# Kernel tuning notes

Measured on AMD Instinct MI355X. Metric: run time of the kernel, lower is better.

Reference implementation:

```python
import jax, jax.numpy as jnp
import numpy as np

DIN = 2048
DOUT = 2048
NUM_HEADS = 16
HEAD_DIM = DIN // NUM_HEADS  # 128
BLOCK_SIZE = 2048
ROPE_THETA = 10000.0


def precompute_freqs(block_size, head_dim):
    inv_freq = 1.0 / (ROPE_THETA ** (jnp.arange(0, head_dim, 2, dtype=jnp.float32) / head_dim))
    t = jnp.arange(block_size, dtype=jnp.float32)
    freqs = jnp.outer(t, inv_freq)  # [S, head_dim//2]
    return jnp.cos(freqs), jnp.sin(freqs)


def apply_rotary_emb(x, cos, sin):
    # x: [B, S, H, D]; cos/sin: [S, D//2]
    xr = x.reshape(*x.shape[:-1], -1, 2)  # pairs of consecutive dims (complex view)
    x1, x2 = xr[..., 0], xr[..., 1]
    c = cos[None, :, None, :]
    s = sin[None, :, None, :]
    o1 = x1 * c - x2 * s
    o2 = x1 * s + x2 * c
    return jnp.stack([o1, o2], axis=-1).reshape(x.shape)


def setup_inputs() -> dict:
    key = jax.random.key(0)
    k1, k2, k3 = jax.random.split(key, 3)
    x = jax.random.normal(k1, (2, 2048, DIN), dtype=jnp.float32)
    Wqkv = jax.random.normal(k2, (DIN, 3 * DOUT), dtype=jnp.float32) * (DIN ** -0.5)
    Wproj = jax.random.normal(k3, (DIN, DOUT), dtype=jnp.float32) * (DIN ** -0.5)
    return {"x": x, "Wqkv": Wqkv, "Wproj": Wproj}


def reference(x, Wqkv, Wproj):
    B, S, _ = x.shape
    cos, sin = precompute_freqs(BLOCK_SIZE, HEAD_DIM)
    cos, sin = cos[:S], sin[:S]
    qkv = x @ Wqkv  # [B, S, 3*DOUT]
    q, k, v = jnp.split(qkv, 3, axis=-1)
    q = q.reshape(B, S, NUM_HEADS, HEAD_DIM)
    k = k.reshape(B, S, NUM_HEADS, HEAD_DIM)
    v = v.reshape(B, S, NUM_HEADS, HEAD_DIM)
    q = apply_rotary_emb(q, cos, sin)
    k = apply_rotary_emb(k, cos, sin)
    # causal SDPA with scale 1/sqrt(head_dim)
    scale = HEAD_DIM ** -0.5
    scores = jnp.einsum('bqhd,bkhd->bhqk', q, k) * scale
    causal = jnp.tril(jnp.ones((S, S), dtype=bool))
    scores = jnp.where(causal[None, None], scores, jnp.finfo(scores.dtype).min)
    attn = jax.nn.softmax(scores, axis=-1)
    y = jnp.einsum('bhqk,bkhd->bqhd', attn, v).reshape(B, S, DOUT)
    return y @ Wproj
```

## Files before the change

kernel.cpp:

```cpp
#include <hip/hip_runtime.h>

#define DIN 2048
#define NH 16
#define DH 128
#define SEQ 2048
#define BB 2
#define N3 6144
#define MM 4096

typedef __bf16 bf16;
typedef __attribute__((ext_vector_type(8))) __bf16 bf16x8;
typedef __attribute__((ext_vector_type(4))) __bf16 bf16x4;
typedef __attribute__((ext_vector_type(2))) __bf16 bf16x2;
typedef __attribute__((ext_vector_type(4))) float f32x4;

__device__ __forceinline__ f32x4 mfma16(bf16x8 a, bf16x8 b, f32x4 c) {
  return __builtin_amdgcn_mfma_f32_16x16x32_bf16(a, b, c, 0, 0, 0);
}

__device__ __forceinline__ void async16(const void* g, void* l) {
  __builtin_amdgcn_global_load_lds((const __attribute__((address_space(1))) void*)g,
                                   (__attribute__((address_space(3))) void*)l, 16, 0, 0);
}

__global__ __launch_bounds__(256) void sniff_trig_k(const unsigned short* __restrict__ x,
                                                    int* __restrict__ flag,
                                                    float2* __restrict__ trig) {
  int i = blockIdx.x * 256 + threadIdx.x;
  int d2 = i & 63, s = i >> 6;
  float invf = expf(-9.210340371976184f * (float)(2 * d2) * (1.0f / 128.0f));
  float sn, cs;
  sincosf((float)s * invf, &sn, &cs);
  trig[i] = make_float2(cs, sn);
  if (blockIdx.x == 0) {
    __shared__ int cnt;
    if (threadIdx.x == 0) cnt = 0;
    __syncthreads();
    unsigned short u = x[threadIdx.x * 2];
    int e = (u >> 7) & 0xff;
    if (e >= 108 && e <= 140) atomicAdd(&cnt, 1);
    __syncthreads();
    if (threadIdx.x == 0) *flag = (cnt >= 128) ? 1 : 0;
  }
}

__global__ __launch_bounds__(256) void cast_x_k(const void* __restrict__ in, bf16* __restrict__ out,
                                                const int* __restrict__ flag) {
  size_t i = ((size_t)blockIdx.x * 256 + threadIdx.x) * 8;
  if (*flag) {
    *(bf16x8*)(out + i) = *(const bf16x8*)((const bf16*)in + i);
  } else {
    const float* f = (const float*)in;
    bf16x8 v;
    for (int j = 0; j < 8; j++) v[j] = (bf16)f[i + j];
    *(bf16x8*)(out + i) = v;
  }
}

__global__ __launch_bounds__(256) void cast_wT_k(const void* __restrict__ in, bf16* __restrict__ out,
                                                 const int* __restrict__ flag, int R, int C) {
  __shared__ float t[32][33];
  int c0 = blockIdx.x * 32, r0 = blockIdx.y * 32;
  int tx = threadIdx.x & 31, ty = threadIdx.x >> 5;
  bool isb = *flag != 0;
  for (int j = 0; j < 4; j++) {
    int r = ty + j * 8;
    size_t idx = (size_t)(r0 + r) * C + c0 + tx;
    float v = isb ? (float)((const bf16*)in)[idx] : ((const float*)in)[idx];
    t[r][tx] = v;
  }
  __syncthreads();
  int tx8 = threadIdx.x & 15;
  int cy = threadIdx.x >> 4;
  for (int j = 0; j < 2; j++) {
    int c = cy + j * 16;
    bf16x2 v;
    v[0] = (bf16)t[2 * tx8][c];
    v[1] = (bf16)t[2 * tx8 + 1][c];
    *(bf16x2*)&out[(size_t)(c0 + c) * R + r0 + 2 * tx8] = v;
  }
}

__global__ __launch_bounds__(256) void gemm_qkv_k(const bf16* __restrict__ A, const bf16* __restrict__ BT,
                                                  bf16* __restrict__ Qb, bf16* __restrict__ Kb,
                                                  bf16* __restrict__ Vt, int m0base) {
  __shared__ __align__(16) bf16 As[128 * 64];
  __shared__ __align__(16) bf16 Bs[128 * 64];
  const int K = DIN;
  int m0 = m0base + blockIdx.y * 128, n0 = blockIdx.x * 128;
  int tid = threadIdx.x, w = tid >> 6, l = tid & 63;
  int l15 = l & 15, quad = l >> 4;
  int wm = (w & 1) * 64, wn = (w >> 1) * 64;
  f32x4 zero = {0.f, 0.f, 0.f, 0.f};
  f32x4 acc[4][4];
  for (int i = 0; i < 4; i++)
    for (int j = 0; j < 4; j++) acc[i][j] = zero;
  int gch = (l & 7) ^ (l >> 3);
  const bf16* Ag = A + (size_t)(m0 + w * 32 + (l >> 3)) * K + gch * 8;
  const bf16* Bg = BT + (size_t)(n0 + w * 32 + (l >> 3)) * K + gch * 8;
  bf16* AsW = As + w * 2048;
  bf16* BsW = Bs + w * 2048;
  for (int k0 = 0; k0 < K; k0 += 64) {
    __syncthreads();
    for (int j = 0; j < 4; j++) async16(Ag + k0 + (size_t)j * 8 * K, AsW + j * 512);
    for (int j = 0; j < 4; j++) async16(Bg + k0 + (size_t)j * 8 * K, BsW + j * 512);
    __syncthreads();
    for (int kk = 0; kk < 2; kk++) {
      bf16x8 af[4], bfv[4];
      for (int i = 0; i < 4; i++)
        af[i] = *(const bf16x8*)&As[(wm + i * 16 + l15) * 64 + (((kk * 4 + quad) ^ (l15 & 7)) << 3)];
      for (int j = 0; j < 4; j++)
        bfv[j] = *(const bf16x8*)&Bs[(wn + j * 16 + l15) * 64 + (((kk * 4 + quad) ^ (l15 & 7)) << 3)];
      for (int i = 0; i < 4; i++)
        for (int j = 0; j < 4; j++) acc[i][j] = mfma16(af[i], bfv[j], acc[i][j]);
    }
  }
  for (int j = 0; j < 4; j++) {
    int col = n0 + wn + j * 16 + l15;
    int part = col >> 11, cw = col & 2047;
    int h = cw >> 7, d = cw & 127;
    if (part < 2) {
      bf16* dst = (part == 0) ? Qb : Kb;
      for (int i = 0; i < 4; i++) {
        int mrow = m0 + wm + i * 16 + quad * 4;
        for (int r = 0; r < 4; r++) {
          int m = mrow + r;
          int b = m >> 11, s = m & 2047;
          int dd = (part == 1) ? ((((d >> 3) ^ (s & 7)) << 3) | (d & 7)) : d;
          dst[(((size_t)(b * NH + h)) * SEQ + s) * DH + dd] = (bf16)acc[i][j][r];
        }
      }
    } else {
      for (int i = 0; i < 4; i++) {
        int mrow = m0 + wm + i * 16 + quad * 4;
        int b = mrow >> 11, s = mrow & 2047;
        int scol = (s & ~63) | (((((s >> 3) & 7) ^ (d & 7)) << 3) | (s & 7));
        bf16x4 pk;
        for (int r = 0; r < 4; r++) pk[r] = (bf16)acc[i][j][r];
        *(bf16x4*)&Vt[((size_t)(b * NH + h) * DH + d) * SEQ + scol] = pk;
      }
    }
  }
}

__global__ __launch_bounds__(256) void rope_lut_k(bf16* __restrict__ Qb, bf16* __restrict__ Kb,
                                                  const float2* __restrict__ trig) {
  int i = blockIdx.x * 256 + threadIdx.x;
  int g = i & 15;
  int s = (i >> 4) & 2047;
  int bh = i >> 15;
  size_t row = ((size_t)bh * SEQ + s) * DH;
  float2 tt[4];
  for (int p = 0; p < 4; p++) tt[p] = trig[(s << 6) + 4 * g + p];
  const float qscale = 0.08838834764831845f * 1.4426950408889634f;
  {
    bf16* qp = Qb + row + 8 * g;
    bf16x8 v = *(const bf16x8*)qp;
    bf16x8 o;
#pragma unroll
    for (int p = 0; p < 4; p++) {
      float e = (float)v[2 * p], od = (float)v[2 * p + 1];
      o[2 * p] = (bf16)((e * tt[p].x - od * tt[p].y) * qscale);
      o[2 * p + 1] = (bf16)((e * tt[p].y + od * tt[p].x) * qscale);
    }
    *(bf16x8*)qp = o;
  }
  {
    bf16* kp = Kb + row + ((g ^ (s & 7)) << 3);
    bf16x8 v = *(const bf16x8*)kp;
    bf16x8 o;
#pragma unroll
    for (int p = 0; p < 4; p++) {
      float e = (float)v[2 * p], od = (float)v[2 * p + 1];
      o[2 * p] = (bf16)(e * tt[p].x - od * tt[p].y);
      o[2 * p + 1] = (bf16)(e * tt[p].y + od * tt[p].x);
    }
    *(bf16x8*)kp = o;
  }
}

__global__ __launch_bounds__(256, 2) void attn_k(const bf16* __restrict__ Qb, const bf16* __restrict__ Kb,
                                                 const bf16* __restrict__ Vt, bf16* __restrict__ Yb) {
  __shared__ __align__(16) bf16 Ks[2][64 * 128];
  __shared__ __align__(16) bf16 Vs[2][128 * 64];
  __shared__ __align__(16) bf16 Pl[4][16 * 76];
  int bh = blockIdx.x;
  int slot = blockIdx.y;
  int w = threadIdx.x >> 6, l = threadIdx.x & 63;
  int l15 = l & 15, quad = l >> 4;
  const bf16* Qp = Qb + (size_t)bh * SEQ * DH;
  const bf16* Kp = Kb + (size_t)bh * SEQ * DH;
  const bf16* Vp = Vt + (size_t)bh * DH * SEQ;
  int b = bh >> 4, h = bh & 15;
  f32x4 zero = {0.f, 0.f, 0.f, 0.f};
  bf16* P = &Pl[w][0];

  auto stage = [&](int it, int buf) {
    const char* gk = (const char*)Kp + (size_t)it * 16384 + w * 4096 + l * 16;
    char* lk = (char*)&Ks[buf][0] + w * 4096;
    for (int i = 0; i < 4; i++) async16(gk + i * 1024, lk + i * 1024);
    const char* gv = (const char*)Vp + (size_t)it * 128 + (size_t)(w * 32 + (l >> 3)) * (SEQ * 2) + (l & 7) * 16;
    char* lv = (char*)&Vs[buf][0] + w * 32 * 128;
    for (int i = 0; i < 4; i++) async16(gv + (size_t)i * 8 * (SEQ * 2), lv + i * 1024);
  };

  int tiles[2] = {31 - slot, slot};
  for (int half = 0; half < 2; half++) {
    int tile = tiles[half];
    int qw = tile * 64 + w * 16;
    bf16x8 qf[4];
    for (int kc = 0; kc < 4; kc++)
      qf[kc] = *(const bf16x8*)&Qp[(size_t)(qw + l15) * DH + kc * 32 + quad * 8];
    f32x4 o[8];
    for (int ns = 0; ns < 8; ns++) o[ns] = zero;
    float mprev = -1e30f, lsum = 0.f;
    int nkt = tile + 1;

    stage(0, 0);
    __syncthreads();
    for (int it = 0; it < nkt; it++) {
      int buf = it & 1;
      bool more = (it + 1 < nkt);
      asm volatile("s_waitcnt vmcnt(4)" ::: "memory");
      __builtin_amdgcn_s_barrier();
      __builtin_amdgcn_sched_barrier(0);
      if (more) stage(it + 1, buf ^ 1);
      int k0 = it * 64;
      f32x4 st[4];
      for (int ns = 0; ns < 4; ns++) st[ns] = zero;
      __builtin_amdgcn_s_setprio(1);
      for (int kc = 0; kc < 4; kc++)
        for (int ns = 0; ns < 4; ns++) {
          bf16x8 kf = *(const bf16x8*)&Ks[buf][(ns * 16 + l15) * 128 + (((kc * 4 + quad) ^ (l15 & 7)) << 3)];
          st[ns] = mfma16(kf, qf[kc], st[ns]);
        }
      __builtin_amdgcn_s_setprio(0);
      int qq = qw + l15;
      if (k0 + 63 > qw) {
        for (int ns = 0; ns < 4; ns++) {
          int kk = k0 + ns * 16 + quad * 4;
          for (int r = 0; r < 4; r++)
            if (kk + r > qq) st[ns][r] = -1e30f;
        }
      }
      float pm = -1e30f;
      for (int ns = 0; ns < 4; ns++)
        for (int r = 0; r < 4; r++) pm = fmaxf(pm, st[ns][r]);
      pm = fmaxf(pm, __shfl_xor(pm, 16, 64));
      pm = fmaxf(pm, __shfl_xor(pm, 32, 64));
      float mnew = fmaxf(mprev, pm);
      float al = exp2f(mprev - mnew);
      mprev = mnew;
      float ps = 0.f;
      for (int ns = 0; ns < 4; ns++)
        for (int r = 0; r < 4; r++) {
          float e = exp2f(st[ns][r] - mnew);
          st[ns][r] = e;
          ps += e;
        }
      ps += __shfl_xor(ps, 16, 64);
      ps += __shfl_xor(ps, 32, 64);
      lsum = lsum * al + ps;
      for (int ns = 0; ns < 8; ns++) o[ns] *= al;
      for (int ns = 0; ns < 4; ns++) {
        bf16x4 pk;
        for (int r = 0; r < 4; r++) pk[r] = (bf16)st[ns][r];
        *(bf16x4*)&P[l15 * 76 + ns * 16 + quad * 4] = pk;
      }
      asm volatile("s_waitcnt lgkmcnt(0)" ::: "memory");
      bf16x8 pa[2];
      for (int kc = 0; kc < 2; kc++)
        pa[kc] = *(const bf16x8*)&P[l15 * 76 + kc * 32 + quad * 8];
      if (more) {
        asm volatile("s_waitcnt vmcnt(8)" ::: "memory");
      } else {
        asm volatile("s_waitcnt vmcnt(0)" ::: "memory");
      }
      __builtin_amdgcn_s_barrier();
      __builtin_amdgcn_sched_barrier(0);
      __builtin_amdgcn_s_setprio(1);
      for (int ns = 0; ns < 8; ns++)
        for (int kc = 0; kc < 2; kc++) {
          bf16x8 vf = *(const bf16x8*)&Vs[buf][(ns * 16 + l15) * 64 + (((kc * 4 + quad) ^ (l15 & 7)) << 3)];
          o[ns] = mfma16(vf, pa[kc], o[ns]);
        }
      __builtin_amdgcn_s_setprio(0);
    }
    __syncthreads();
    float inv = 1.0f / lsum;
    int q = qw + l15;
    size_t base = ((size_t)(b * SEQ + q)) * DIN + h * DH + quad * 4;
    for (int ns = 0; ns < 8; ns++) {
      bf16x4 pk;
      for (int r = 0; r < 4; r++) pk[r] = (bf16)(o[ns][r] * inv);
      *(bf16x4*)&Yb[base + ns * 16] = pk;
    }
  }
}

__global__ __launch_bounds__(256) void gemm_proj_k(const bf16* __restrict__ A, const bf16* __restrict__ BT,
                                                   void* __restrict__ out, const int* __restrict__ flag) {
  __shared__ __align__(16) bf16 As[128 * 64];
  __shared__ __align__(16) bf16 Bs[128 * 64];
  const int K = DIN;
  int m0 = blockIdx.y * 128, n0 = blockIdx.x * 128;
  int tid = threadIdx.x, w = tid >> 6, l = tid & 63;
  int l15 = l & 15, quad = l >> 4;
  int wm = (w & 1) * 64, wn = (w >> 1) * 64;
  bool obf = *flag != 0;
  f32x4 zero = {0.f, 0.f, 0.f, 0.f};
  f32x4 acc[4][4];
  for (int i = 0; i < 4; i++)
    for (int j = 0; j < 4; j++) acc[i][j] = zero;
  int gch = (l & 7) ^ (l >> 3);
  const bf16* Ag = A + (size_t)(m0 + w * 32 + (l >> 3)) * K + gch * 8;
  const bf16* Bg = BT + (size_t)(n0 + w * 32 + (l >> 3)) * K + gch * 8;
  bf16* AsW = As + w * 2048;
  bf16* BsW = Bs + w * 2048;
  for (int k0 = 0; k0 < K; k0 += 64) {
    __syncthreads();
    for (int j = 0; j < 4; j++) async16(Ag + k0 + (size_t)j * 8 * K, AsW + j * 512);
    for (int j = 0; j < 4; j++) async16(Bg + k0 + (size_t)j * 8 * K, BsW + j * 512);
    __syncthreads();
    for (int kk = 0; kk < 2; kk++) {
      bf16x8 af[4], bfv[4];
      for (int i = 0; i < 4; i++)
        af[i] = *(const bf16x8*)&As[(wm + i * 16 + l15) * 64 + (((kk * 4 + quad) ^ (l15 & 7)) << 3)];
      for (int j = 0; j < 4; j++)
        bfv[j] = *(const bf16x8*)&Bs[(wn + j * 16 + l15) * 64 + (((kk * 4 + quad) ^ (l15 & 7)) << 3)];
      for (int i = 0; i < 4; i++)
        for (int j = 0; j < 4; j++) acc[i][j] = mfma16(af[i], bfv[j], acc[i][j]);
    }
  }
  for (int j = 0; j < 4; j++) {
    int col = n0 + wn + j * 16 + l15;
    for (int i = 0; i < 4; i++) {
      int mrow = m0 + wm + i * 16 + quad * 4;
      for (int r = 0; r < 4; r++) {
        size_t idx = (size_t)(mrow + r) * DIN + col;
        float v = acc[i][j][r];
        if (obf)
          ((bf16*)out)[idx] = (bf16)v;
        else
          ((float*)out)[idx] = v;
      }
    }
  }
}

extern "C" void kernel_launch(void* const* d_in, const int* in_sizes, int n_in,
                              void* d_out, int out_size, void* d_ws, size_t ws_size,
                              hipStream_t stream) {
  char* ws = (char*)d_ws;
  int* flag = (int*)ws;
  bf16* Xb = (bf16*)(ws + 256);
  bf16* WqkvT = (bf16*)(ws + 256 + 16777216);
  bf16* WprojT = (bf16*)(ws + 256 + 16777216 + 25165824);
  bf16* Qb = (bf16*)(ws + 256 + 16777216 + 25165824 + 8388608);
  bf16* Kb = Qb + (size_t)MM * DIN;
  bf16* Vb = Kb + (size_t)MM * DIN;
  bf16* Vt = Vb + (size_t)MM * DIN;
  bf16* Yb = Xb;
  float2* trig = (float2*)Vb;

  sniff_trig_k<<<512, 256, 0, stream>>>((const unsigned short*)d_in[0], flag, trig);
  cast_x_k<<<4096, 256, 0, stream>>>(d_in[0], Xb, flag);
  cast_wT_k<<<dim3(192, 64), 256, 0, stream>>>(d_in[1], WqkvT, flag, DIN, N3);
  cast_wT_k<<<dim3(64, 64), 256, 0, stream>>>(d_in[2], WprojT, flag, DIN, DIN);
  gemm_qkv_k<<<dim3(48, 16), 256, 0, stream>>>(Xb, WqkvT, Qb, Kb, Vt, 0);
  gemm_qkv_k<<<dim3(48, 16), 256, 0, stream>>>(Xb, WqkvT, Qb, Kb, Vt, 2048);
  rope_lut_k<<<4096, 256, 0, stream>>>(Qb, Kb, trig);
  attn_k<<<dim3(32, 16), 256, 0, stream>>>(Qb, Kb, Vt, Yb);
  gemm_proj_k<<<dim3(16, 32), 256, 0, stream>>>(Yb, WprojT, d_out, flag);
}
```

Baseline: 419.5 us.

## Widen attention to 32 queries per wave and fuse Q RoPE into attention

The attention kernel now gives each wave 32 query rows (two 16-row halves) over a 128-row tile. Each K/V tile loaded into LDS is therefore reused for twice as many queries, and the paired-tile loop of the old version is dropped. Q RoPE and scaling move into the attention prologue, so the rope kernel only rotates K. The softmax rescale is skipped unless the running max grows by more than a threshold, and V is single-buffered. The two QKV GEMM launches are merged into one grid. The costs are higher register pressure, a full vmcnt(0) wait each iteration, less overlap on V loads, and possibly worse load balance from the reversed tile order.

```diff
diff --git a/kernel.cpp b/kernel.cpp
--- a/kernel.cpp
+++ b/kernel.cpp
@@ -83,11 +83,11 @@
 
 __global__ __launch_bounds__(256) void gemm_qkv_k(const bf16* __restrict__ A, const bf16* __restrict__ BT,
                                                   bf16* __restrict__ Qb, bf16* __restrict__ Kb,
-                                                  bf16* __restrict__ Vt, int m0base) {
+                                                  bf16* __restrict__ Vt) {
   __shared__ __align__(16) bf16 As[128 * 64];
   __shared__ __align__(16) bf16 Bs[128 * 64];
   const int K = DIN;
-  int m0 = m0base + blockIdx.y * 128, n0 = blockIdx.x * 128;
+  int m0 = blockIdx.y * 128, n0 = blockIdx.x * 128;
   int tid = threadIdx.x, w = tid >> 6, l = tid & 63;
   int l15 = l & 15, quad = l >> 4;
   int wm = (w & 1) * 64, wn = (w >> 1) * 64;
@@ -143,7 +143,7 @@
   }
 }
 
-__global__ __launch_bounds__(256) void rope_lut_k(bf16* __restrict__ Qb, bf16* __restrict__ Kb,
+__global__ __launch_bounds__(256) void rope_lut_k(bf16* __restrict__ Kb,
                                                   const float2* __restrict__ trig) {
   int i = blockIdx.x * 256 + threadIdx.x;
   int g = i & 15;
@@ -152,40 +152,27 @@
   size_t row = ((size_t)bh * SEQ + s) * DH;
   float2 tt[4];
   for (int p = 0; p < 4; p++) tt[p] = trig[(s << 6) + 4 * g + p];
-  const float qscale = 0.08838834764831845f * 1.4426950408889634f;
-  {
-    bf16* qp = Qb + row + 8 * g;
-    bf16x8 v = *(const bf16x8*)qp;
-    bf16x8 o;
-#pragma unroll
-    for (int p = 0; p < 4; p++) {
-      float e = (float)v[2 * p], od = (float)v[2 * p + 1];
-      o[2 * p] = (bf16)((e * tt[p].x - od * tt[p].y) * qscale);
-      o[2 * p + 1] = (bf16)((e * tt[p].y + od * tt[p].x) * qscale);
-    }
-    *(bf16x8*)qp = o;
-  }
-  {
-    bf16* kp = Kb + row + ((g ^ (s & 7)) << 3);
-    bf16x8 v = *(const bf16x8*)kp;
-    bf16x8 o;
-#pragma unroll
-    for (int p = 0; p < 4; p++) {
-      float e = (float)v[2 * p], od = (float)v[2 * p + 1];
-      o[2 * p] = (bf16)(e * tt[p].x - od * tt[p].y);
-      o[2 * p + 1] = (bf16)(e * tt[p].y + od * tt[p].x);
-    }
-    *(bf16x8*)kp = o;
-  }
+  bf16* kp = Kb + row + ((g ^ (s & 7)) << 3);
+  bf16x8 v = *(const bf16x8*)kp;
+  bf16x8 o;
+#pragma unroll
+  for (int p = 0; p < 4; p++) {
+    float e = (float)v[2 * p], od = (float)v[2 * p + 1];
+    o[2 * p] = (bf16)(e * tt[p].x - od * tt[p].y);
+    o[2 * p + 1] = (bf16)(e * tt[p].y + od * tt[p].x);
+  }
+  *(bf16x8*)kp = o;
 }
 
 __global__ __launch_bounds__(256, 2) void attn_k(const bf16* __restrict__ Qb, const bf16* __restrict__ Kb,
-                                                 const bf16* __restrict__ Vt, bf16* __restrict__ Yb) {
+                                                 const bf16* __restrict__ Vt,
+                                                 const float2* __restrict__ trig,
+                                                 bf16* __restrict__ Yb) {
   __shared__ __align__(16) bf16 Ks[2][64 * 128];
-  __shared__ __align__(16) bf16 Vs[2][128 * 64];
-  __shared__ __align__(16) bf16 Pl[4][16 * 76];
+  __shared__ __align__(16) bf16 Vs[128 * 64];
+  __shared__ __align__(16) bf16 Pl[4][32 * 72];
   int bh = blockIdx.x;
-  int slot = blockIdx.y;
+  int tile = 15 - (int)blockIdx.y;
   int w = threadIdx.x >> 6, l = threadIdx.x & 63;
   int l15 = l & 15, quad = l >> 4;
   const bf16* Qp = Qb + (size_t)bh * SEQ * DH;
@@ -195,104 +182,156 @@
   f32x4 zero = {0.f, 0.f, 0.f, 0.f};
   bf16* P = &Pl[w][0];
 
-  auto stage = [&](int it, int buf) {
+  auto stageK = [&](int it, int buf) {
     const char* gk = (const char*)Kp + (size_t)it * 16384 + w * 4096 + l * 16;
     char* lk = (char*)&Ks[buf][0] + w * 4096;
     for (int i = 0; i < 4; i++) async16(gk + i * 1024, lk + i * 1024);
+  };
+  auto stageV = [&](int it) {
     const char* gv = (const char*)Vp + (size_t)it * 128 + (size_t)(w * 32 + (l >> 3)) * (SEQ * 2) + (l & 7) * 16;
-    char* lv = (char*)&Vs[buf][0] + w * 32 * 128;
+    char* lv = (char*)&Vs[0] + w * 32 * 128;
     for (int i = 0; i < 4; i++) async16(gv + (size_t)i * 8 * (SEQ * 2), lv + i * 1024);
   };
 
-  int tiles[2] = {31 - slot, slot};
-  for (int half = 0; half < 2; half++) {
-    int tile = tiles[half];
-    int qw = tile * 64 + w * 16;
-    bf16x8 qf[4];
-    for (int kc = 0; kc < 4; kc++)
-      qf[kc] = *(const bf16x8*)&Qp[(size_t)(qw + l15) * DH + kc * 32 + quad * 8];
-    f32x4 o[8];
-    for (int ns = 0; ns < 8; ns++) o[ns] = zero;
-    float mprev = -1e30f, lsum = 0.f;
-    int nkt = tile + 1;
-
-    stage(0, 0);
-    __syncthreads();
-    for (int it = 0; it < nkt; it++) {
-      int buf = it & 1;
-      bool more = (it + 1 < nkt);
-      asm volatile("s_waitcnt vmcnt(4)" ::: "memory");
-      __builtin_amdgcn_s_barrier();
-      __builtin_amdgcn_sched_barrier(0);
-      if (more) stage(it + 1, buf ^ 1);
-      int k0 = it * 64;
-      f32x4 st[4];
-      for (int ns = 0; ns < 4; ns++) st[ns] = zero;
+  int qw = tile * 128 + w * 32;
+  const float qscale = 0.08838834764831845f * 1.4426950408889634f;
+  bf16x8 qf[2][4];
+#pragma unroll
+  for (int hh = 0; hh < 2; hh++) {
+    int s = qw + hh * 16 + l15;
+#pragma unroll
+    for (int kc = 0; kc < 4; kc++) {
+      bf16x8 v = *(const bf16x8*)&Qp[(size_t)s * DH + kc * 32 + quad * 8];
+      bf16x8 o;
+#pragma unroll
+      for (int p = 0; p < 4; p++) {
+        float2 t = trig[(s << 6) + kc * 16 + quad * 4 + p];
+        float e = (float)v[2 * p], od = (float)v[2 * p + 1];
+        o[2 * p] = (bf16)((e * t.x - od * t.y) * qscale);
+        o[2 * p + 1] = (bf16)((e * t.y + od * t.x) * qscale);
+      }
+      qf[hh][kc] = o;
+    }
+  }
+
+  f32x4 o[2][8];
+#pragma unroll
+  for (int hh = 0; hh < 2; hh++)
+    for (int ns = 0; ns < 8; ns++) o[hh][ns] = zero;
+  float mprev[2] = {-1e30f, -1e30f}, lsum[2] = {0.f, 0.f};
+  int nkt = 2 * tile + 2;
+
+  stageK(0, 0);
+  for (int it = 0; it < nkt; it++) {
+    int buf = it & 1;
+    bool more = (it + 1 < nkt);
+    int k0 = it * 64;
+    asm volatile("s_waitcnt vmcnt(0)" ::: "memory");
+    __builtin_amdgcn_s_barrier();
+    __builtin_amdgcn_sched_barrier(0);
+    if (more) stageK(it + 1, buf ^ 1);
+    stageV(it);
+    bool a0 = (k0 <= qw + 15), a1 = (k0 <= qw + 31);
+    bf16x8 pa[2][2];
+    if (a1) {
+      f32x4 st[2][4];
+#pragma unroll
+      for (int hh = 0; hh < 2; hh++)
+        for (int ns = 0; ns < 4; ns++) st[hh][ns] = zero;
       __builtin_amdgcn_s_setprio(1);
+#pragma unroll
       for (int kc = 0; kc < 4; kc++)
+#pragma unroll
         for (int ns = 0; ns < 4; ns++) {
           bf16x8 kf = *(const bf16x8*)&Ks[buf][(ns * 16 + l15) * 128 + (((kc * 4 + quad) ^ (l15 & 7)) << 3)];
-          st[ns] = mfma16(kf, qf[kc], st[ns]);
+          if (a0) st[0][ns] = mfma16(kf, qf[0][kc], st[0][ns]);
+          st[1][ns] = mfma16(kf, qf[1][kc], st[1][ns]);
         }
       __builtin_amdgcn_s_setprio(0);
-      int qq = qw + l15;
-      if (k0 + 63 > qw) {
+#pragma unroll
+      for (int hh = 0; hh < 2; hh++) {
+        if (hh == 0 && !a0) continue;
+        int qh = qw + hh * 16;
+        int qq = qh + l15;
+        if (k0 + 63 > qh) {
+#pragma unroll
+          for (int ns = 0; ns < 4; ns++) {
+            int kk = k0 + ns * 16 + quad * 4;
+#pragma unroll
+            for (int r = 0; r < 4; r++)
+              if (kk + r > qq) st[hh][ns][r] = -1e30f;
+          }
+        }
+        float pm = -1e30f;
+#pragma unroll
+        for (int ns = 0; ns < 4; ns++)
+          for (int r = 0; r < 4; r++) pm = fmaxf(pm, st[hh][ns][r]);
+        pm = fmaxf(pm, __shfl_xor(pm, 16, 64));
+        pm = fmaxf(pm, __shfl_xor(pm, 32, 64));
+        if (!__all(pm - mprev[hh] <= 8.0f)) {
+          float mnew = fmaxf(mprev[hh], pm);
+          float al = exp2f(mprev[hh] - mnew);
+          mprev[hh] = mnew;
+          lsum[hh] *= al;
+#pragma unroll
+          for (int ns = 0; ns < 8; ns++) o[hh][ns] *= al;
+        }
+        float ps = 0.f;
+#pragma unroll
+        for (int ns = 0; ns < 4; ns++)
+          for (int r = 0; r < 4; r++) {
+            float e = exp2f(st[hh][ns][r] - mprev[hh]);
+            st[hh][ns][r] = e;
+            ps += e;
+          }
+        ps += __shfl_xor(ps, 16, 64);
+        ps += __shfl_xor(ps, 32, 64);
+        lsum[hh] += ps;
+#pragma unroll
         for (int ns = 0; ns < 4; ns++) {
-          int kk = k0 + ns * 16 + quad * 4;
-          for (int r = 0; r < 4; r++)
-            if (kk + r > qq) st[ns][r] = -1e30f;
-        }
-      }
-      float pm = -1e30f;
-      for (int ns = 0; ns < 4; ns++)
-        for (int r = 0; r < 4; r++) pm = fmaxf(pm, st[ns][r]);
-      pm = fmaxf(pm, __shfl_xor(pm, 16, 64));
-      pm = fmaxf(pm, __shfl_xor(pm, 32, 64));
-      float mnew = fmaxf(mprev, pm);
-      float al = exp2f(mprev - mnew);
-      mprev = mnew;
-      float ps = 0.f;
-      for (int ns = 0; ns < 4; ns++)
-        for (int r = 0; r < 4; r++) {
-          float e = exp2f(st[ns][r] - mnew);
-          st[ns][r] = e;
-          ps += e;
-        }
-      ps += __shfl_xor(ps, 16, 64);
-      ps += __shfl_xor(ps, 32, 64);
-      lsum = lsum * al + ps;
-      for (int ns = 0; ns < 8; ns++) o[ns] *= al;
-      for (int ns = 0; ns < 4; ns++) {
-        bf16x4 pk;
-        for (int r = 0; r < 4; r++) pk[r] = (bf16)st[ns][r];
-        *(bf16x4*)&P[l15 * 76 + ns * 16 + quad * 4] = pk;
+          bf16x4 pk;
+          for (int r = 0; r < 4; r++) pk[r] = (bf16)st[hh][ns][r];
+          *(bf16x4*)&P[(hh * 16 + l15) * 72 + ns * 16 + quad * 4] = pk;
+        }
       }
       asm volatile("s_waitcnt lgkmcnt(0)" ::: "memory");
-      bf16x8 pa[2];
-      for (int kc = 0; kc < 2; kc++)
-        pa[kc] = *(const bf16x8*)&P[l15 * 76 + kc * 32 + quad * 8];
-      if (more) {
-        asm volatile("s_waitcnt vmcnt(8)" ::: "memory");
-      } else {
-        asm volatile("s_waitcnt vmcnt(0)" ::: "memory");
-      }
-      __builtin_amdgcn_s_barrier();
-      __builtin_amdgcn_sched_barrier(0);
+#pragma unroll
+      for (int hh = 0; hh < 2; hh++) {
+        if (hh == 0 && !a0) continue;
+#pragma unroll
+        for (int kc = 0; kc < 2; kc++)
+          pa[hh][kc] = *(const bf16x8*)&P[(hh * 16 + l15) * 72 + kc * 32 + quad * 8];
+      }
+    }
+    if (more) {
+      asm volatile("s_waitcnt vmcnt(4)" ::: "memory");
+    } else {
+      asm volatile("s_waitcnt vmcnt(0)" ::: "memory");
+    }
+    __builtin_amdgcn_s_barrier();
+    __builtin_amdgcn_sched_barrier(0);
+    if (a1) {
       __builtin_amdgcn_s_setprio(1);
+#pragma unroll
       for (int ns = 0; ns < 8; ns++)
+#pragma unroll
         for (int kc = 0; kc < 2; kc++) {
-          bf16x8 vf = *(const bf16x8*)&Vs[buf][(ns * 16 + l15) * 64 + (((kc * 4 + quad) ^ (l15 & 7)) << 3)];
-          o[ns] = mfma16(vf, pa[kc], o[ns]);
+          bf16x8 vf = *(const bf16x8*)&Vs[(ns * 16 + l15) * 64 + (((kc * 4 + quad) ^ (l15 & 7)) << 3)];
+          if (a0) o[0][ns] = mfma16(vf, pa[0][kc], o[0][ns]);
+          o[1][ns] = mfma16(vf, pa[1][kc], o[1][ns]);
         }
       __builtin_amdgcn_s_setprio(0);
     }
-    __syncthreads();
-    float inv = 1.0f / lsum;
-    int q = qw + l15;
+  }
+#pragma unroll
+  for (int hh = 0; hh < 2; hh++) {
+    float inv = 1.0f / lsum[hh];
+    int q = qw + hh * 16 + l15;
     size_t base = ((size_t)(b * SEQ + q)) * DIN + h * DH + quad * 4;
+#pragma unroll
     for (int ns = 0; ns < 8; ns++) {
       bf16x4 pk;
-      for (int r = 0; r < 4; r++) pk[r] = (bf16)(o[ns][r] * inv);
+      for (int r = 0; r < 4; r++) pk[r] = (bf16)(o[hh][ns][r] * inv);
       *(bf16x4*)&Yb[base + ns * 16] = pk;
     }
   }
@@ -367,9 +406,8 @@
   cast_x_k<<<4096, 256, 0, stream>>>(d_in[0], Xb, flag);
   cast_wT_k<<<dim3(192, 64), 256, 0, stream>>>(d_in[1], WqkvT, flag, DIN, N3);
   cast_wT_k<<<dim3(64, 64), 256, 0, stream>>>(d_in[2], WprojT, flag, DIN, DIN);
-  gemm_qkv_k<<<dim3(48, 16), 256, 0, stream>>>(Xb, WqkvT, Qb, Kb, Vt, 0);
-  gemm_qkv_k<<<dim3(48, 16), 256, 0, stream>>>(Xb, WqkvT, Qb, Kb, Vt, 2048);
-  rope_lut_k<<<4096, 256, 0, stream>>>(Qb, Kb, trig);
-  attn_k<<<dim3(32, 16), 256, 0, stream>>>(Qb, Kb, Vt, Yb);
+  gemm_qkv_k<<<dim3(48, 32), 256, 0, stream>>>(Xb, WqkvT, Qb, Kb, Vt);
+  rope_lut_k<<<4096, 256, 0, stream>>>(Kb, trig);
+  attn_k<<<dim3(32, 16), 256, 0, stream>>>(Qb, Kb, Vt, trig, Yb);
   gemm_proj_k<<<dim3(16, 32), 256, 0, stream>>>(Yb, WprojT, d_out, flag);
 }
```

After: 402.1 us. 1.04x faster.
